# Performance work log

Hardware: AMD Instinct MI355X
Metric: run time of the kernel (lower is better)

## Reference

```python
import jax, jax.numpy as jnp
import numpy as np

B, T, D = 32, 512, 1024  # batch, timesteps, features == units (residual add requires D == units)


def _layer_norm(x, gamma, beta, eps=1e-3):  # Keras LayerNormalization default eps=1e-3, axis=-1
    m = jnp.mean(x, axis=-1, keepdims=True)
    v = jnp.var(x, axis=-1, keepdims=True)
    return (x - m) * jax.lax.rsqrt(v + eps) * gamma + beta


def setup_inputs() -> dict:
    key = jax.random.key(0)
    ks = jax.random.split(key, 4)
    units = D
    # unit_forget_bias=True: forget-gate bias initialized to ones (gate order i, f, c, o)
    bias = jnp.concatenate([jnp.zeros((units,)), jnp.ones((units,)), jnp.zeros((2 * units,))]).astype(jnp.float32)
    return {
        "x": jax.random.normal(ks[0], (B, T, D), dtype=jnp.float32),
        "ln1_gamma": jnp.ones((D,), jnp.float32),
        "ln1_beta": jnp.zeros((D,), jnp.float32),
        "kernel": jax.random.normal(ks[1], (D, 4 * units), dtype=jnp.float32) * 0.02,
        "recurrent_kernel": jax.random.normal(ks[2], (units, 4 * units), dtype=jnp.float32) * 0.02,
        "bias": bias,
        "ln2_gamma": jnp.ones((D,), jnp.float32),
        "ln2_beta": jnp.zeros((D,), jnp.float32),
    }


def reference(x, ln1_gamma, ln1_beta, kernel, recurrent_kernel, bias, ln2_gamma, ln2_beta):
    xn = _layer_norm(x, ln1_gamma, ln1_beta)
    units = recurrent_kernel.shape[0]

    def step(carry, xt):  # xt: [B, D]
        h, c = carry
        z = xt @ kernel + h @ recurrent_kernel + bias  # [B, 4U]
        i, f, g, o = jnp.split(z, 4, axis=-1)  # Keras gate order i, f, c~, o
        c_new = jax.nn.sigmoid(f) * c + jax.nn.sigmoid(i) * jnp.tanh(g)
        h_new = jax.nn.sigmoid(o) * jnp.tanh(c_new)
        return (h_new, c_new), None

    h0 = jnp.zeros((x.shape[0], units), x.dtype)
    (h_last, _), _ = jax.lax.scan(step, (h0, h0), jnp.swapaxes(xn, 0, 1))  # scan over T
    # Keras RNN (return_sequences=False) yields only the final hidden state [B, U];
    # dropout is identity at inference; Add broadcasts it over the time axis.
    out = _layer_norm(xn + h_last[:, None, :], ln2_gamma, ln2_beta)
    return out
```

## Files before the change

kernel.cpp:

```cpp
#include <hip/hip_runtime.h>

typedef unsigned short u16;
typedef unsigned int   u32;
typedef unsigned long long u64;
typedef __attribute__((ext_vector_type(8)))  short  short8v;
typedef __attribute__((ext_vector_type(4)))  float  f32x4;
typedef __attribute__((ext_vector_type(16))) float  f32x16;
typedef __attribute__((ext_vector_type(4)))  unsigned short ushort4v;
typedef __attribute__((ext_vector_type(4)))  u32 u32x4;

#define B_   32
#define T_   512
#define D_   1024
#define N4_  4096
#define NWG  128

#define OFF_XN   0ull
#define OFF_ZX   33554432ull
#define OFF_KT   167772160ull
#define OFF_RT   176160768ull
#define OFF_HB   184549376ull
#define OFF_FLG  184680448ull

__device__ inline u16 f2bf(float f) {
  union { float f; u32 u; } x; x.f = f;
  u32 r = x.u + 0x7FFFu + ((x.u >> 16) & 1u);
  return (u16)(r >> 16);
}
__device__ inline float bf2f(u16 h) {
  union { u32 u; float f; } x; x.u = ((u32)h) << 16; return x.f;
}
__device__ inline float sigm(float x) { return 1.f / (1.f + __expf(-x)); }
__device__ inline float tanh_fast(float x) {
  float e = __expf(2.f * x);
  return 1.f - 2.f / (e + 1.f);
}

__global__ __launch_bounds__(256) void init_kernel(u32* hbuf, u32* flags) {
  int i = blockIdx.x * 256 + threadIdx.x;
  if (i < 32768) hbuf[i] = 0u;
  if (i < NWG)   flags[i * 16] = 0u;
}

__global__ __launch_bounds__(256) void ln1_kernel(const float* __restrict__ x,
    const float* __restrict__ gam, const float* __restrict__ bet, u16* __restrict__ xn) {
  int row = blockIdx.x; int tid = threadIdx.x;
  const float* xr = x + (size_t)row * D_;
  float4 v = *(const float4*)(xr + tid * 4);
  float s  = v.x + v.y + v.z + v.w;
  float ss = v.x*v.x + v.y*v.y + v.z*v.z + v.w*v.w;
  #pragma unroll
  for (int o = 32; o > 0; o >>= 1) { s += __shfl_down(s, o); ss += __shfl_down(ss, o); }
  __shared__ float red[8];
  int w = tid >> 6, l = tid & 63;
  if (l == 0) { red[w] = s; red[4 + w] = ss; }
  __syncthreads();
  s  = red[0] + red[1] + red[2] + red[3];
  ss = red[4] + red[5] + red[6] + red[7];
  float mean = s * (1.f / D_);
  float var  = ss * (1.f / D_) - mean * mean;
  float rstd = rsqrtf(var + 1e-3f);
  float4 g = *(const float4*)(gam + tid * 4);
  float4 b = *(const float4*)(bet + tid * 4);
  ushort4v o4;
  o4.x = f2bf((v.x - mean) * rstd * g.x + b.x);
  o4.y = f2bf((v.y - mean) * rstd * g.y + b.y);
  o4.z = f2bf((v.z - mean) * rstd * g.z + b.z);
  o4.w = f2bf((v.w - mean) * rstd * g.w + b.w);
  *(ushort4v*)(xn + (size_t)row * D_ + tid * 4) = o4;
}

__global__ __launch_bounds__(256) void transpose_bf16(const float* __restrict__ W, u16* __restrict__ WT) {
  __shared__ float tile[32][33];
  int c0 = blockIdx.x * 32, r0 = blockIdx.y * 32;
  int tx = threadIdx.x, ty = threadIdx.y;
  #pragma unroll
  for (int i = ty; i < 32; i += 8)
    tile[i][tx] = W[(size_t)(r0 + i) * N4_ + c0 + tx];
  __syncthreads();
  #pragma unroll
  for (int i = ty; i < 32; i += 8)
    WT[(size_t)(c0 + i) * D_ + r0 + tx] = f2bf(tile[tx][i]);
}

__global__ __launch_bounds__(256) void gemm_xk(const u16* __restrict__ A, const u16* __restrict__ Bt,
    const float* __restrict__ bias, u16* __restrict__ Zx) {
  __shared__ u16 As[128 * 32];
  __shared__ u16 Bs[128 * 32];
  int tid = threadIdx.x;
  int bm = blockIdx.x >> 5, bn = blockIdx.x & 31;
  int w = tid >> 6, l = tid & 63;
  int srow = tid >> 2, sk = (tid & 3) * 8;
  const u16* Ag = A  + (size_t)(bm * 128 + srow) * D_ + sk;
  const u16* Bg = Bt + (size_t)(bn * 128 + srow) * D_ + sk;
  int sb0 = (srow * 64 + sk * 2)          ^ ((srow & 3) << 4);
  int sb1 = ((srow + 64) * 64 + sk * 2)   ^ ((srow & 3) << 4);
  int wm = w >> 1, wn = w & 1;
  int frow = l & 15, fko = (l >> 4) * 16;
  f32x4 acc[4][4];
  #pragma unroll
  for (int mi = 0; mi < 4; ++mi)
    #pragma unroll
    for (int ni = 0; ni < 4; ++ni)
      #pragma unroll
      for (int j = 0; j < 4; ++j) acc[mi][ni][j] = 0.f;

  short8v ap0 = *(const short8v*)(Ag);
  short8v ap1 = *(const short8v*)(Ag + 64 * (size_t)D_);
  short8v bp0 = *(const short8v*)(Bg);
  short8v bp1 = *(const short8v*)(Bg + 64 * (size_t)D_);

  for (int kt = 0; kt < 32; ++kt) {
    __syncthreads();
    *(short8v*)((char*)As + sb0) = ap0;
    *(short8v*)((char*)As + sb1) = ap1;
    *(short8v*)((char*)Bs + sb0) = bp0;
    *(short8v*)((char*)Bs + sb1) = bp1;
    __syncthreads();
    if (kt < 31) {
      ap0 = *(const short8v*)(Ag + (kt + 1) * 32);
      ap1 = *(const short8v*)(Ag + 64 * (size_t)D_ + (kt + 1) * 32);
      bp0 = *(const short8v*)(Bg + (kt + 1) * 32);
      bp1 = *(const short8v*)(Bg + 64 * (size_t)D_ + (kt + 1) * 32);
    }
    short8v af[4], bfr[4];
    #pragma unroll
    for (int mi = 0; mi < 4; ++mi) {
      int r = wm * 64 + mi * 16 + frow;
      af[mi] = *(const short8v*)((char*)As + ((r * 64 + fko) ^ ((r & 3) << 4)));
    }
    #pragma unroll
    for (int ni = 0; ni < 4; ++ni) {
      int r = wn * 64 + ni * 16 + frow;
      bfr[ni] = *(const short8v*)((char*)Bs + ((r * 64 + fko) ^ ((r & 3) << 4)));
    }
    #pragma unroll
    for (int mi = 0; mi < 4; ++mi)
      #pragma unroll
      for (int ni = 0; ni < 4; ++ni)
        acc[mi][ni] = __builtin_amdgcn_mfma_f32_16x16x32_bf16(af[mi], bfr[ni], acc[mi][ni], 0, 0, 0);
  }
  #pragma unroll
  for (int mi = 0; mi < 4; ++mi) {
    #pragma unroll
    for (int ni = 0; ni < 4; ++ni) {
      int col = bn * 128 + wn * 64 + ni * 16 + (l & 15);
      float bv = bias[col];
      int colp = ((col & 1023) << 2) | (col >> 10);
      #pragma unroll
      for (int j = 0; j < 4; ++j) {
        int row = bm * 128 + wm * 64 + mi * 16 + (l >> 4) * 4 + j;
        int zrow = (row & 511) * 32 + (row >> 9);
        Zx[(size_t)zrow * N4_ + colp] = f2bf(acc[mi][ni][j] + bv);
      }
    }
  }
}

__global__ __launch_bounds__(512) __attribute__((amdgpu_waves_per_eu(2, 2)))
void lstm_scan(const u16* __restrict__ Zx,
    const u16* __restrict__ RT, u16* hbuf, float* h_last, u32* flags) {
  __shared__ u16   h_lds[B_ * D_];
  __shared__ float z_lds[8 * 32 * 36];
  int tid = threadIdx.x;
  int wg = blockIdx.x;
  int w = tid >> 6, l = tid & 63;
  int ks = w;
  int bcol = l & 31, hi = l >> 5;

  short8v b[8];
  {
    const u16* Rp = RT + (size_t)((bcol & 3) * 1024 + wg * 8 + (bcol >> 2)) * D_
                  + ks * 128 + hi * 8;
    #pragma unroll
    for (int kt = 0; kt < 8; ++kt) b[kt] = *(const short8v*)(Rp + kt * 16);
  }
  #pragma unroll
  for (int kt = 0; kt < 8; ++kt) asm volatile("" : "+v"(b[kt]));

  int abase = bcol * 2048 + ks * 256 + hi * 16;
  int asw = (bcol & 7) << 4;
  int grow = tid >> 3, gu = tid & 7;
  const u16* zx_p = Zx + (size_t)grow * N4_ + (wg * 8 + gu) * 4;
  int hoff = grow * D_ + wg * 8 + gu;
  float c = 0.f;
  const u32* fp0 = flags + (size_t)l * 16;
  const u32* fp1 = flags + (size_t)(64 + l) * 16;

  #pragma unroll 1
  for (int t = 0; t < T_; ++t) {
    u64 zq = 0;
    if (tid < 256) zq = *(const u64*)(zx_p + (size_t)t * B_ * N4_);
    __builtin_amdgcn_sched_barrier(0);

    if (w == 0) {
      while (true) {
        u32 f0 = __hip_atomic_load(fp0, __ATOMIC_RELAXED, __HIP_MEMORY_SCOPE_AGENT);
        u32 f1 = __hip_atomic_load(fp1, __ATOMIC_RELAXED, __HIP_MEMORY_SCOPE_AGENT);
        if (__all((int)(f0 >= (u32)t && f1 >= (u32)t))) break;
      }
    }
    __builtin_amdgcn_s_barrier();
    __builtin_amdgcn_sched_barrier(0);

    const char* hbp = (const char*)hbuf + (size_t)(t & 1) * 65536;
    u32x4 hv[8];
    #pragma unroll
    for (int j = 0; j < 8; ++j) {
      const char* p = hbp + j * 8192 + tid * 16;
      asm volatile("global_load_dwordx4 %0, %1, off sc0 sc1"
                   : "=&v"(hv[j]) : "v"(p) : "memory");
    }
    asm volatile("s_waitcnt vmcnt(0)" ::: "memory");
    __builtin_amdgcn_sched_barrier(0);
    #pragma unroll
    for (int j = 0; j < 8; ++j) {
      int byte = j * 8192 + tid * 16;
      int row = byte >> 11;
      *(u32x4*)((char*)h_lds + (byte ^ ((row & 7) << 4))) = hv[j];
    }
    __syncthreads();

    f32x16 acc;
    #pragma unroll
    for (int i = 0; i < 16; ++i) acc[i] = 0.f;
    #pragma unroll
    for (int kt = 0; kt < 8; ++kt) {
      short8v a = *(const short8v*)((const char*)h_lds + ((abase + kt * 32) ^ asw));
      acc = __builtin_amdgcn_mfma_f32_32x32x16_bf16(a, b[kt], acc, 0, 0, 0);
    }
    #pragma unroll
    for (int r = 0; r < 16; ++r) {
      int rowD = (r & 3) + 8 * (r >> 2) + 4 * hi;
      z_lds[(ks * 32 + rowD) * 36 + bcol] = acc[r];
    }
    __syncthreads();

    if (tid < 256) {
      float z0 = bf2f((u16)(zq        & 0xFFFFu));
      float z1 = bf2f((u16)((zq >> 16) & 0xFFFFu));
      float z2 = bf2f((u16)((zq >> 32) & 0xFFFFu));
      float z3 = bf2f((u16)((zq >> 48) & 0xFFFFu));
      #pragma unroll
      for (int kss = 0; kss < 8; ++kss) {
        f32x4 zr = *(const f32x4*)&z_lds[(kss * 32 + grow) * 36 + gu * 4];
        z0 += zr[0]; z1 += zr[1]; z2 += zr[2]; z3 += zr[3];
      }
      float cn = sigm(z1) * c + sigm(z0) * tanh_fast(z2);
      float hn = sigm(z3) * tanh_fast(cn);
      c = cn;

      u32 hw = (u32)f2bf(hn);
      u32 nb = __shfl_down(hw, 1);
      if (!(gu & 1)) {
        u32* dst = (u32*)(hbuf + (size_t)((t + 1) & 1) * (B_ * D_) + hoff);
        __hip_atomic_store(dst, hw | (nb << 16), __ATOMIC_RELAXED, __HIP_MEMORY_SCOPE_AGENT);
      }
      if (t == T_ - 1) h_last[hoff] = hn;
    }
    __syncthreads();
    if (tid == 0)
      __hip_atomic_store(flags + (size_t)wg * 16, (u32)(t + 1),
                         __ATOMIC_RELAXED, __HIP_MEMORY_SCOPE_AGENT);
  }
}

__global__ __launch_bounds__(256) void ln2_kernel(const u16* __restrict__ xn,
    const float* __restrict__ h_last, const float* __restrict__ gam,
    const float* __restrict__ bet, float* __restrict__ out) {
  int row = blockIdx.x; int tid = threadIdx.x;
  int bi = row >> 9;
  ushort4v xv = *(const ushort4v*)(xn + (size_t)row * D_ + tid * 4);
  float4 hv = *(const float4*)(h_last + (size_t)bi * D_ + tid * 4);
  float s0 = bf2f(xv.x) + hv.x;
  float s1 = bf2f(xv.y) + hv.y;
  float s2 = bf2f(xv.z) + hv.z;
  float s3 = bf2f(xv.w) + hv.w;
  float s = s0 + s1 + s2 + s3;
  float ss = s0*s0 + s1*s1 + s2*s2 + s3*s3;
  #pragma unroll
  for (int o = 32; o > 0; o >>= 1) { s += __shfl_down(s, o); ss += __shfl_down(ss, o); }
  __shared__ float red[8];
  int w = tid >> 6, l = tid & 63;
  if (l == 0) { red[w] = s; red[4 + w] = ss; }
  __syncthreads();
  s  = red[0] + red[1] + red[2] + red[3];
  ss = red[4] + red[5] + red[6] + red[7];
  float mean = s * (1.f / D_);
  float var  = ss * (1.f / D_) - mean * mean;
  float rstd = rsqrtf(var + 1e-3f);
  float4 g = *(const float4*)(gam + tid * 4);
  float4 b = *(const float4*)(bet + tid * 4);
  float4 o4;
  o4.x = (s0 - mean) * rstd * g.x + b.x;
  o4.y = (s1 - mean) * rstd * g.y + b.y;
  o4.z = (s2 - mean) * rstd * g.z + b.z;
  o4.w = (s3 - mean) * rstd * g.w + b.w;
  *(float4*)(out + (size_t)row * D_ + tid * 4) = o4;
}

extern "C" void kernel_launch(void* const* d_in, const int* in_sizes, int n_in,
                              void* d_out, int out_size, void* d_ws, size_t ws_size,
                              hipStream_t stream) {
  const float* x    = (const float*)d_in[0];
  const float* g1   = (const float*)d_in[1];
  const float* b1   = (const float*)d_in[2];
  const float* Wk   = (const float*)d_in[3];
  const float* Wr   = (const float*)d_in[4];
  const float* bias = (const float*)d_in[5];
  const float* g2   = (const float*)d_in[6];
  const float* b2   = (const float*)d_in[7];
  char* ws = (char*)d_ws;
  u16* xn    = (u16*)(ws + OFF_XN);
  u16* Zx    = (u16*)(ws + OFF_ZX);
  u16* KT    = (u16*)(ws + OFF_KT);
  u16* RT    = (u16*)(ws + OFF_RT);
  u16* hbuf  = (u16*)(ws + OFF_HB);
  u32* flg   = (u32*)(ws + OFF_FLG);
  float* hl  = (float*)(ws + OFF_KT);
  float* out = (float*)d_out;

  init_kernel<<<128, 256, 0, stream>>>((u32*)hbuf, flg);
  ln1_kernel<<<B_ * T_, 256, 0, stream>>>(x, g1, b1, xn);
  transpose_bf16<<<dim3(128, 32), dim3(32, 8), 0, stream>>>(Wk, KT);
  transpose_bf16<<<dim3(128, 32), dim3(32, 8), 0, stream>>>(Wr, RT);
  gemm_xk<<<4096, 256, 0, stream>>>(xn, KT, bias, Zx);
  lstm_scan<<<NWG, 512, 0, stream>>>(Zx, RT, hbuf, hl, flg);
  ln2_kernel<<<B_ * T_, 256, 0, stream>>>(xn, hl, g2, b2, out);
}
```

Before: 1.643 ms.

## Split LSTM recurrent scan across batch halves with 256 workgroups and 16x16 MFMA

The persistent recurrent scan now runs on 256 workgroups instead of 128, and each pair of workgroups shares a unit slice while splitting the batch into two halves of 16 rows. Each workgroup loads half as much hidden state per step and switches from 32x32x16 to two 16x16x32 MFMAs per k-tile. The goal is to halve per-step h loading and matmul latency on the serial critical path. In exchange, every barrier poll has to check twice as many flags, and the grid needs 256 co-resident workgroups.

```diff
diff --git a/kernel.cpp b/kernel.cpp
--- a/kernel.cpp
+++ b/kernel.cpp
@@ -5,7 +5,6 @@
 typedef unsigned long long u64;
 typedef __attribute__((ext_vector_type(8)))  short  short8v;
 typedef __attribute__((ext_vector_type(4)))  float  f32x4;
-typedef __attribute__((ext_vector_type(16))) float  f32x16;
 typedef __attribute__((ext_vector_type(4)))  unsigned short ushort4v;
 typedef __attribute__((ext_vector_type(4)))  u32 u32x4;
 
@@ -13,7 +12,7 @@
 #define T_   512
 #define D_   1024
 #define N4_  4096
-#define NWG  128
+#define NWG  256
 
 #define OFF_XN   0ull
 #define OFF_ZX   33554432ull
@@ -160,53 +159,64 @@
 __global__ __launch_bounds__(512) __attribute__((amdgpu_waves_per_eu(2, 2)))
 void lstm_scan(const u16* __restrict__ Zx,
     const u16* __restrict__ RT, u16* hbuf, float* h_last, u32* flags) {
-  __shared__ u16   h_lds[B_ * D_];
-  __shared__ float z_lds[8 * 32 * 36];
+  __shared__ u16   h_lds[16 * D_];
+  __shared__ float z_lds[8 * 16 * 36];
   int tid = threadIdx.x;
   int wg = blockIdx.x;
+  int ug = wg >> 1, bh = wg & 1;
   int w = tid >> 6, l = tid & 63;
   int ks = w;
-  int bcol = l & 31, hi = l >> 5;
-
-  short8v b[8];
-  {
-    const u16* Rp = RT + (size_t)((bcol & 3) * 1024 + wg * 8 + (bcol >> 2)) * D_
+  int fr = l & 15, hi = l >> 4;
+
+  short8v b[4][2];
+  #pragma unroll
+  for (int ch = 0; ch < 2; ++ch) {
+    int c = ch * 16 + fr;
+    const u16* Rp = RT + (size_t)((c & 3) * 1024 + ug * 8 + (c >> 2)) * D_
                   + ks * 128 + hi * 8;
     #pragma unroll
-    for (int kt = 0; kt < 8; ++kt) b[kt] = *(const short8v*)(Rp + kt * 16);
-  }
-  #pragma unroll
-  for (int kt = 0; kt < 8; ++kt) asm volatile("" : "+v"(b[kt]));
-
-  int abase = bcol * 2048 + ks * 256 + hi * 16;
-  int asw = (bcol & 7) << 4;
+    for (int kt = 0; kt < 4; ++kt) b[kt][ch] = *(const short8v*)(Rp + kt * 32);
+  }
+  #pragma unroll
+  for (int kt = 0; kt < 4; ++kt) {
+    asm volatile("" : "+v"(b[kt][0]));
+    asm volatile("" : "+v"(b[kt][1]));
+  }
+
+  int abase = fr * 2048 + ks * 256 + hi * 16;
+  int asw = (fr & 7) << 4;
   int grow = tid >> 3, gu = tid & 7;
-  const u16* zx_p = Zx + (size_t)grow * N4_ + (wg * 8 + gu) * 4;
-  int hoff = grow * D_ + wg * 8 + gu;
+  const u16* zx_p = Zx + (size_t)(bh * 16 + grow) * N4_ + (ug * 8 + gu) * 4;
+  int hoff = (bh * 16 + grow) * D_ + ug * 8 + gu;
   float c = 0.f;
   const u32* fp0 = flags + (size_t)l * 16;
   const u32* fp1 = flags + (size_t)(64 + l) * 16;
+  const u32* fp2 = flags + (size_t)(128 + l) * 16;
+  const u32* fp3 = flags + (size_t)(192 + l) * 16;
 
   #pragma unroll 1
   for (int t = 0; t < T_; ++t) {
     u64 zq = 0;
-    if (tid < 256) zq = *(const u64*)(zx_p + (size_t)t * B_ * N4_);
+    if (tid < 128) zq = *(const u64*)(zx_p + (size_t)t * B_ * N4_);
     __builtin_amdgcn_sched_barrier(0);
 
     if (w == 0) {
       while (true) {
         u32 f0 = __hip_atomic_load(fp0, __ATOMIC_RELAXED, __HIP_MEMORY_SCOPE_AGENT);
         u32 f1 = __hip_atomic_load(fp1, __ATOMIC_RELAXED, __HIP_MEMORY_SCOPE_AGENT);
-        if (__all((int)(f0 >= (u32)t && f1 >= (u32)t))) break;
+        u32 f2 = __hip_atomic_load(fp2, __ATOMIC_RELAXED, __HIP_MEMORY_SCOPE_AGENT);
+        u32 f3 = __hip_atomic_load(fp3, __ATOMIC_RELAXED, __HIP_MEMORY_SCOPE_AGENT);
+        u32 t32 = (u32)t;
+        if (__all((int)(f0 >= t32 && f1 >= t32 && f2 >= t32 && f3 >= t32))) break;
       }
     }
     __builtin_amdgcn_s_barrier();
     __builtin_amdgcn_sched_barrier(0);
 
-    const char* hbp = (const char*)hbuf + (size_t)(t & 1) * 65536;
-    u32x4 hv[8];
-    #pragma unroll
-    for (int j = 0; j < 8; ++j) {
+    const char* hbp = (const char*)hbuf + (size_t)(t & 1) * 65536 + (size_t)bh * 32768;
+    u32x4 hv[4];
+    #pragma unroll
+    for (int j = 0; j < 4; ++j) {
       const char* p = hbp + j * 8192 + tid * 16;
       asm volatile("global_load_dwordx4 %0, %1, off sc0 sc1"
                    : "=&v"(hv[j]) : "v"(p) : "memory");
@@ -214,36 +224,38 @@
     asm volatile("s_waitcnt vmcnt(0)" ::: "memory");
     __builtin_amdgcn_sched_barrier(0);
     #pragma unroll
-    for (int j = 0; j < 8; ++j) {
+    for (int j = 0; j < 4; ++j) {
       int byte = j * 8192 + tid * 16;
       int row = byte >> 11;
       *(u32x4*)((char*)h_lds + (byte ^ ((row & 7) << 4))) = hv[j];
     }
     __syncthreads();
 
-    f32x16 acc;
-    #pragma unroll
-    for (int i = 0; i < 16; ++i) acc[i] = 0.f;
-    #pragma unroll
-    for (int kt = 0; kt < 8; ++kt) {
-      short8v a = *(const short8v*)((const char*)h_lds + ((abase + kt * 32) ^ asw));
-      acc = __builtin_amdgcn_mfma_f32_32x32x16_bf16(a, b[kt], acc, 0, 0, 0);
-    }
-    #pragma unroll
-    for (int r = 0; r < 16; ++r) {
-      int rowD = (r & 3) + 8 * (r >> 2) + 4 * hi;
-      z_lds[(ks * 32 + rowD) * 36 + bcol] = acc[r];
-    }
-    __syncthreads();
-
-    if (tid < 256) {
+    f32x4 acc0, acc1;
+    #pragma unroll
+    for (int i = 0; i < 4; ++i) { acc0[i] = 0.f; acc1[i] = 0.f; }
+    #pragma unroll
+    for (int kt = 0; kt < 4; ++kt) {
+      short8v a = *(const short8v*)((const char*)h_lds + ((abase + kt * 64) ^ asw));
+      acc0 = __builtin_amdgcn_mfma_f32_16x16x32_bf16(a, b[kt][0], acc0, 0, 0, 0);
+      acc1 = __builtin_amdgcn_mfma_f32_16x16x32_bf16(a, b[kt][1], acc1, 0, 0, 0);
+    }
+    #pragma unroll
+    for (int j = 0; j < 4; ++j) {
+      int rowD = hi * 4 + j;
+      z_lds[(ks * 16 + rowD) * 36 + fr]      = acc0[j];
+      z_lds[(ks * 16 + rowD) * 36 + 16 + fr] = acc1[j];
+    }
+    __syncthreads();
+
+    if (tid < 128) {
       float z0 = bf2f((u16)(zq        & 0xFFFFu));
       float z1 = bf2f((u16)((zq >> 16) & 0xFFFFu));
       float z2 = bf2f((u16)((zq >> 32) & 0xFFFFu));
       float z3 = bf2f((u16)((zq >> 48) & 0xFFFFu));
       #pragma unroll
       for (int kss = 0; kss < 8; ++kss) {
-        f32x4 zr = *(const f32x4*)&z_lds[(kss * 32 + grow) * 36 + gu * 4];
+        f32x4 zr = *(const f32x4*)&z_lds[(kss * 16 + grow) * 36 + gu * 4];
         z0 += zr[0]; z1 += zr[1]; z2 += zr[2]; z3 += zr[3];
       }
       float cn = sigm(z1) * c + sigm(z0) * tanh_fast(z2);
```

Result: faster. 1.568 ms (-4.6%).
